# Kernel optimization log

Measured on AMD Instinct MI355X. Metric: run time of the kernel, lower is better.

Reference implementation:

```python
import jax, jax.numpy as jnp
import numpy as np

N_NODES = 50000
N_EDGES = 800000
IN_C, HID_C, OUT_C = 128, 128, 40


def gcn_conv(x, W, b, src, dst, dinv):
    # x: [N, Fin] -> [N, Fout]; PyG GCNConv: h = W x, then sym-normalized
    # aggregation over edges (incl. self-loops), plus bias.
    h = x @ W  # [N, Fout]
    norm = dinv[src] * dinv[dst]  # [E+N]
    msg = h[src] * norm[:, None]  # gather + scale, [E+N, Fout]
    out = jax.ops.segment_sum(msg, dst, num_segments=x.shape[0])
    return out + b


def _prep_edges(edge_index, n):
    # add self-loops; compute deg^{-1/2} with unit edge weights
    loop = jnp.arange(n, dtype=edge_index.dtype)
    src = jnp.concatenate([edge_index[0], loop])
    dst = jnp.concatenate([edge_index[1], loop])
    deg = jax.ops.segment_sum(jnp.ones_like(dst, dtype=jnp.float32), dst, num_segments=n)
    dinv = jnp.where(deg > 0, jax.lax.rsqrt(jnp.maximum(deg, 1.0)), 0.0)
    return src, dst, dinv


def setup_inputs() -> dict:
    key = jax.random.key(0)
    ks = jax.random.split(key, 5)
    x = jax.random.normal(ks[0], (N_NODES, IN_C), dtype=jnp.float32)
    edge_index = jax.random.randint(ks[1], (2, N_EDGES), 0, N_NODES, dtype=jnp.int32)
    s = 0.05
    W1 = jax.random.normal(ks[2], (IN_C, HID_C), dtype=jnp.float32) * s
    W2 = jax.random.normal(ks[3], (HID_C, HID_C), dtype=jnp.float32) * s
    W3 = jax.random.normal(ks[4], (HID_C, OUT_C), dtype=jnp.float32) * s
    return {
        "x": x, "edge_index": edge_index,
        "W1": W1, "b1": jnp.zeros((HID_C,), jnp.float32),
        "W2": W2, "b2": jnp.zeros((HID_C,), jnp.float32),
        "W3": W3, "b3": jnp.zeros((OUT_C,), jnp.float32),
    }


def reference(x, edge_index, W1, b1, W2, b2, W3, b3):
    n = x.shape[0]
    src, dst, dinv = _prep_edges(edge_index, n)
    h = jax.nn.relu(gcn_conv(x, W1, b1, src, dst, dinv))  # dropout = id (eval)
    h = jax.nn.relu(gcn_conv(h, W2, b2, src, dst, dinv))
    h = gcn_conv(h, W3, b3, src, dst, dinv)
    return jax.nn.log_softmax(h, axis=1)
```

## Files before the change

### kernel.cpp

```cpp
#include <hip/hip_runtime.h>
#include <cmath>

__device__ __forceinline__ unsigned short f2bf(float f) {
  unsigned u = __float_as_uint(f);
  u = (u + 0x7FFFu + ((u >> 16) & 1u)) >> 16;
  return (unsigned short)u;
}
__device__ __forceinline__ unsigned pack2(float a, float b) {
  return (unsigned)f2bf(a) | ((unsigned)f2bf(b) << 16);
}
__device__ __forceinline__ float bflo(unsigned u) { return __uint_as_float(u << 16); }
__device__ __forceinline__ float bfhi(unsigned u) { return __uint_as_float(u & 0xFFFF0000u); }
__device__ __forceinline__ float bf1(unsigned short h) { return __uint_as_float((unsigned)h << 16); }

__device__ __forceinline__ unsigned char fp8e(float v) {
  unsigned u = __float_as_uint(v * 0x1.0p-120f);
  unsigned s = (u >> 24) & 0x80u;
  u &= 0x7FFFFFFFu;
  u = u + 0x000FFFFFu + ((u >> 20) & 1u);
  return (unsigned char)(s | ((u >> 20) & 0x7Fu));
}
__device__ __forceinline__ float fp8d(unsigned b) {
  unsigned u = ((b & 0x80u) << 24) | ((b & 0x7Fu) << 20);
  return __uint_as_float(u) * 0x1.0p120f;
}

typedef float f32x2 __attribute__((ext_vector_type(2)));

#if defined(__has_builtin)
#if __has_builtin(__builtin_amdgcn_cvt_pk_f32_fp8)
#define HW_FP8 1
#endif
#endif

__device__ __forceinline__ void fp8d4(unsigned v, float4& acc) {
#ifdef HW_FP8
  f32x2 lo = __builtin_amdgcn_cvt_pk_f32_fp8((int)v, false);
  f32x2 hi = __builtin_amdgcn_cvt_pk_f32_fp8((int)v, true);
  acc.x += lo[0]; acc.y += lo[1]; acc.z += hi[0]; acc.w += hi[1];
#else
  acc.x += fp8d(v & 0xFF);
  acc.y += fp8d((v >> 8) & 0xFF);
  acc.z += fp8d((v >> 16) & 0xFF);
  acc.w += fp8d(v >> 24);
#endif
}

using bh8 = __attribute__((ext_vector_type(8))) short;
using f32x4 = __attribute__((ext_vector_type(4))) float;

#define BK_STRIDE 8192

__global__ __launch_bounds__(256) void k_bin(const int* __restrict__ src, const int* __restrict__ dst,
                                             int* __restrict__ bucketCur, unsigned* __restrict__ bucketBuf,
                                             int E, int chunk,
                                             const float* __restrict__ W1, const float* __restrict__ W2,
                                             const float* __restrict__ W3, unsigned short* __restrict__ Wt1,
                                             unsigned short* __restrict__ Wt2, unsigned short* __restrict__ Wt3) {
  __shared__ int hist[256], base[256], cur[256];
  int t = threadIdx.x;
  hist[t] = 0;
  cur[t] = 0;
  __syncthreads();
  int s0 = blockIdx.x * chunk;
  int s1 = min(E, s0 + chunk);
  for (int i = s0 + t; i < s1; i += 256) atomicAdd(&hist[dst[i] >> 8], 1);
  __syncthreads();
  if (hist[t] > 0) base[t] = atomicAdd(&bucketCur[t], hist[t]);
  __syncthreads();
  for (int i = s0 + t; i < s1; i += 256) {
    int d = dst[i];
    int b = d >> 8;
    int r = base[b] + atomicAdd(&cur[b], 1);
    if (r < BK_STRIDE)
      bucketBuf[(size_t)b * BK_STRIDE + r] = (unsigned)src[i] | ((unsigned)(d & 255) << 16);
  }
  int tid = blockIdx.x * 256 + t;
  int stride = gridDim.x * 256;
  for (int i = tid; i < 32768 + 6144; i += stride) {
    if (i < 16384) {
      int c = i >> 7, k = i & 127;
      Wt1[i] = f2bf(W1[(size_t)k * 128 + c]);
    } else if (i < 32768) {
      int j = i - 16384;
      int c = j >> 7, k = j & 127;
      Wt2[j] = f2bf(W2[(size_t)k * 128 + c]);
    } else {
      int j = i - 32768;
      int c = j >> 7, k = j & 127;
      Wt3[j] = (c < 40) ? f2bf(W3[(size_t)k * 40 + c]) : (unsigned short)0;
    }
  }
}

__global__ __launch_bounds__(256) void k_build(const unsigned* __restrict__ bucketBuf,
                                               const int* __restrict__ bucketCnt, int* __restrict__ rp,
                                               float* __restrict__ dinv, int* __restrict__ csr, int n, int nbk) {
  __shared__ int hist[256], excl[256], cur[256], s[256], bc[256];
  int b = blockIdx.x, t = threadIdx.x;
  int bv = (t < nbk) ? bucketCnt[t] : 0;
  bc[t] = bv;
  s[t] = bv;
  __syncthreads();
  for (int off = 1; off < 256; off <<= 1) {
    int u = (t >= off) ? s[t - off] : 0;
    __syncthreads();
    s[t] += u;
    __syncthreads();
  }
  int e0 = s[b] - bc[b];
  int cntE = bc[b];
  int Etot = s[nbk - 1];
  __syncthreads();
  const unsigned* buf = bucketBuf + (size_t)b * BK_STRIDE;
  hist[t] = 0;
  cur[t] = 0;
  __syncthreads();
  for (int i = t; i < cntE; i += 256) atomicAdd(&hist[(buf[i] >> 16) & 255], 1);
  __syncthreads();
  int h = hist[t];
  s[t] = h;
  __syncthreads();
  for (int off = 1; off < 256; off <<= 1) {
    int u = (t >= off) ? s[t - off] : 0;
    __syncthreads();
    s[t] += u;
    __syncthreads();
  }
  excl[t] = s[t] - h;
  int node = (b << 8) + t;
  if (node < n) {
    rp[node] = e0 + excl[t];
    dinv[node] = rsqrtf((float)(h + 1));
  }
  if (b == nbk - 1 && t == 0) rp[n] = Etot;
  __syncthreads();
  for (int i = t; i < cntE; i += 256) {
    unsigned p = buf[i];
    int lo = (p >> 16) & 255;
    int r = atomicAdd(&cur[lo], 1);
    csr[e0 + excl[lo] + r] = (int)(p & 0xFFFFu);
  }
}

template <int WT_N, int NW_COL, int MOUT, bool OUT8, bool A32>
__global__ __launch_bounds__(256) void k_mfma_gemm(const void* __restrict__ Av,
                                                   const unsigned short* __restrict__ Bt,
                                                   const float* __restrict__ dinv,
                                                   void* __restrict__ Gv, int n) {
  constexpr int NW_ROW = 4 / NW_COL;
  int tid = threadIdx.x;
  int wid = tid >> 6, lane = tid & 63;
  int lr = lane & 15, lq = lane >> 4;
  int wrow = wid / NW_COL, wcol = wid % NW_COL;
  int rowBase = blockIdx.x * (NW_ROW * 32) + wrow * 32;
  int colBase = wcol * (WT_N * 16);

  bh8 af[2][4];
#pragma unroll
  for (int rt = 0; rt < 2; rt++) {
    int row = rowBase + rt * 16 + lr;
    bool ok = row < n;
    if constexpr (A32) {
      const float* ap = (const float*)Av + (size_t)row * 128 + lq * 8;
#pragma unroll
      for (int ks = 0; ks < 4; ks++) {
        union { uint4 u; bh8 h; } w;
        if (ok) {
          float4 v0 = *(const float4*)(ap + ks * 32);
          float4 v1 = *(const float4*)(ap + ks * 32 + 4);
          w.u = make_uint4(pack2(v0.x, v0.y), pack2(v0.z, v0.w), pack2(v1.x, v1.y), pack2(v1.z, v1.w));
        } else {
          w.u = make_uint4(0u, 0u, 0u, 0u);
        }
        af[rt][ks] = w.h;
      }
    } else {
      const unsigned short* ap = (const unsigned short*)Av + (size_t)row * 128 + lq * 8;
#pragma unroll
      for (int ks = 0; ks < 4; ks++) {
        bh8 z = {0, 0, 0, 0, 0, 0, 0, 0};
        af[rt][ks] = ok ? *(const bh8*)(ap + ks * 32) : z;
      }
    }
  }
  bh8 bfr[WT_N][4];
#pragma unroll
  for (int ct = 0; ct < WT_N; ct++) {
    const unsigned short* bp = Bt + (size_t)(colBase + ct * 16 + lr) * 128 + lq * 8;
#pragma unroll
    for (int ks = 0; ks < 4; ks++) bfr[ct][ks] = *(const bh8*)(bp + ks * 32);
  }

  f32x4 acc[2][WT_N];
#pragma unroll
  for (int rt = 0; rt < 2; rt++)
#pragma unroll
    for (int ct = 0; ct < WT_N; ct++) acc[rt][ct] = (f32x4){0.f, 0.f, 0.f, 0.f};

#pragma unroll
  for (int ks = 0; ks < 4; ks++)
#pragma unroll
    for (int rt = 0; rt < 2; rt++)
#pragma unroll
      for (int ct = 0; ct < WT_N; ct++)
        acc[rt][ct] = __builtin_amdgcn_mfma_f32_16x16x32_bf16(af[rt][ks], bfr[ct][ks], acc[rt][ct], 0, 0, 0);

#pragma unroll
  for (int rt = 0; rt < 2; rt++)
#pragma unroll
    for (int r = 0; r < 4; r++) {
      int row = rowBase + rt * 16 + lq * 4 + r;
      if (row < n) {
        float di = dinv[row];
#pragma unroll
        for (int ct = 0; ct < WT_N; ct++) {
          int col = colBase + ct * 16 + lr;
          if (MOUT == 128 || col < MOUT) {
            if constexpr (OUT8)
              ((unsigned char*)Gv)[(size_t)row * MOUT + col] = fp8e(acc[rt][ct][r] * di);
            else
              ((unsigned short*)Gv)[(size_t)row * MOUT + col] = f2bf(acc[rt][ct][r] * di);
          }
        }
      }
    }
}

__global__ __launch_bounds__(256) void k_agg_relu128_f8(const unsigned char* __restrict__ g8,
                                                        const int* __restrict__ csr, const int* __restrict__ rp,
                                                        const float* __restrict__ dinv, const float* __restrict__ bias,
                                                        unsigned short* __restrict__ out, int n) {
  int t = threadIdx.x;
  int node = blockIdx.x * 8 + (t >> 5);
  if (node >= n) return;
  int c = t & 31;
  const unsigned* g32 = (const unsigned*)g8;
  int e0 = rp[node], e1 = rp[node + 1];

  float4 a[8];
#pragma unroll
  for (int u = 0; u < 8; u++) a[u] = make_float4(0.f, 0.f, 0.f, 0.f);
  fp8d4(g32[(size_t)node * 32 + c], a[0]);

  int e = e0;
  for (; e + 8 <= e1; e += 8) {
    int s[8];
#pragma unroll
    for (int u = 0; u < 8; u++) s[u] = csr[e + u];
    unsigned v[8];
#pragma unroll
    for (int u = 0; u < 8; u++) v[u] = g32[(size_t)s[u] * 32 + c];
#pragma unroll
    for (int u = 0; u < 8; u++) fp8d4(v[u], a[u]);
  }
  for (; e < e1; ++e) fp8d4(g32[(size_t)csr[e] * 32 + c], a[0]);

#pragma unroll
  for (int u = 4; u < 8; u++) {
    a[u - 4].x += a[u].x; a[u - 4].y += a[u].y; a[u - 4].z += a[u].z; a[u - 4].w += a[u].w;
  }
#pragma unroll
  for (int u = 2; u < 4; u++) {
    a[u - 2].x += a[u].x; a[u - 2].y += a[u].y; a[u - 2].z += a[u].z; a[u - 2].w += a[u].w;
  }
  float4 acc = make_float4(a[0].x + a[1].x, a[0].y + a[1].y, a[0].z + a[1].z, a[0].w + a[1].w);

  float di = dinv[node];
  float4 bb = *(const float4*)&bias[c * 4];
  uint2 o;
  o.x = pack2(fmaxf(fmaf(di, acc.x, bb.x), 0.f), fmaxf(fmaf(di, acc.y, bb.y), 0.f));
  o.y = pack2(fmaxf(fmaf(di, acc.z, bb.z), 0.f), fmaxf(fmaf(di, acc.w, bb.w), 0.f));
  *(uint2*)&out[(size_t)node * 128 + c * 4] = o;
}

__global__ __launch_bounds__(256) void k_agg_lsm40_f8(const unsigned char* __restrict__ g8,
                                                      const int* __restrict__ csr, const int* __restrict__ rp,
                                                      const float* __restrict__ dinv, const float* __restrict__ bias,
                                                      float* __restrict__ out, int n) {
  int lane = threadIdx.x & 63;
  int node = blockIdx.x * 4 + (threadIdx.x >> 6);
  if (node >= n) return;
  int e0 = rp[node], e1 = rp[node + 1];

  float a[8];
  a[0] = fp8d(g8[(size_t)node * 40 + lane]);
#pragma unroll
  for (int u = 1; u < 8; u++) a[u] = 0.f;

  int e = e0;
  for (; e + 8 <= e1; e += 8) {
    int s[8];
#pragma unroll
    for (int u = 0; u < 8; u++) s[u] = csr[e + u];
#pragma unroll
    for (int u = 0; u < 8; u++) a[u] += fp8d(g8[(size_t)s[u] * 40 + lane]);
  }
  for (; e < e1; ++e) a[0] += fp8d(g8[(size_t)csr[e] * 40 + lane]);

  float acc = ((a[0] + a[1]) + (a[2] + a[3])) + ((a[4] + a[5]) + (a[6] + a[7]));

  bool act = lane < 40;
  float v = act ? fmaf(dinv[node], acc, bias[lane]) : -INFINITY;
  float m = v;
#pragma unroll
  for (int off = 32; off > 0; off >>= 1) m = fmaxf(m, __shfl_xor(m, off, 64));
  float ex = act ? __expf(v - m) : 0.f;
  float ssum = ex;
#pragma unroll
  for (int off = 32; off > 0; off >>= 1) ssum += __shfl_xor(ssum, off, 64);
  if (act) out[(size_t)node * 40 + lane] = v - m - __logf(ssum);
}


extern "C" void kernel_launch(void* const* d_in, const int* in_sizes, int n_in,
                              void* d_out, int out_size, void* d_ws, size_t ws_size,
                              hipStream_t stream) {
  const float* x  = (const float*)d_in[0];
  const int*   ei = (const int*)d_in[1];
  const float* W1 = (const float*)d_in[2];
  const float* b1 = (const float*)d_in[3];
  const float* W2 = (const float*)d_in[4];
  const float* b2 = (const float*)d_in[5];
  const float* W3 = (const float*)d_in[6];
  const float* b3 = (const float*)d_in[7];
  float* out = (float*)d_out;
  int n = in_sizes[0] / 128;
  int E = in_sizes[1] / 2;
  const int* esrc = ei;
  const int* edst = ei + E;
  int nbk = (n + 255) >> 8;

  size_t off = 0;
  auto alloc = [&](size_t bytes) -> void* {
    void* r = (char*)d_ws + off;
    off += (bytes + 255) & ~(size_t)255;
    return r;
  };
  int*      bucketCur  = (int*)alloc(256 * 4);
  unsigned* bucketBuf  = (unsigned*)alloc((size_t)nbk * BK_STRIDE * 4);
  int*      rp         = (int*)alloc((size_t)(n + 1) * 4);
  float*    dinv       = (float*)alloc((size_t)n * 4);
  int*      csr        = (int*)alloc((size_t)E * 4);
  unsigned short* bufB = (unsigned short*)alloc((size_t)n * 128 * 2 + 4096);
  unsigned short* bufC = (unsigned short*)alloc((size_t)n * 128 * 2 + 4096);
  unsigned char*  gq   = (unsigned char*)alloc((size_t)n * 128 + 4096);
  unsigned short* Wt1  = (unsigned short*)alloc(128 * 128 * 2);
  unsigned short* Wt2  = (unsigned short*)alloc(128 * 128 * 2);
  unsigned short* Wt3  = (unsigned short*)alloc(48 * 128 * 2);

  hipMemsetAsync(bucketCur, 0, 256 * 4, stream);

  const int BIN_BLOCKS = 512;
  int chunk = (E + BIN_BLOCKS - 1) / BIN_BLOCKS;
  k_bin<<<BIN_BLOCKS, 256, 0, stream>>>(esrc, edst, bucketCur, bucketBuf, E, chunk, W1, W2, W3, Wt1, Wt2, Wt3);
  k_build<<<nbk, 256, 0, stream>>>(bucketBuf, bucketCur, rp, dinv, csr, n, nbk);

  k_mfma_gemm<4, 2, 128, true, true><<<(n + 63) / 64, 256, 0, stream>>>(x, Wt1, dinv, gq, n);
  k_agg_relu128_f8<<<(n + 7) / 8, 256, 0, stream>>>(gq, csr, rp, dinv, b1, bufB, n);
  k_mfma_gemm<4, 2, 128, true, false><<<(n + 63) / 64, 256, 0, stream>>>(bufB, Wt2, dinv, gq, n);
  k_agg_relu128_f8<<<(n + 7) / 8, 256, 0, stream>>>(gq, csr, rp, dinv, b2, bufC, n);
  k_mfma_gemm<3, 1, 40, true, false><<<(n + 127) / 128, 256, 0, stream>>>(bufC, Wt3, dinv, gq, n);
  k_agg_lsm40_f8<<<(n + 3) / 4, 256, 0, stream>>>(gq, csr, rp, dinv, b3, out, n);
}
```

Baseline: 180.8 us.

## Fuse aggregation with next-layer GEMM via LDS staging

Merges each layer's neighbour aggregation (bias and ReLU) with the following layer's MFMA GEMM. Each block aggregates 32 nodes into a padded LDS tile and multiplies it by the weight tile, so the bf16 hidden activations no longer go to global memory and two launches are removed. In exchange each block now does a serial gather phase followed by a GEMM phase with a barrier between them, and in the 40-column layer one of four waves sits idle during the GEMM, which may cost latency hiding.

After: 190.8 us. +5.5%, slower.

```diff
diff --git a/kernel.cpp b/kernel.cpp
--- a/kernel.cpp
+++ b/kernel.cpp
@@ -9,8 +9,6 @@
 __device__ __forceinline__ unsigned pack2(float a, float b) {
   return (unsigned)f2bf(a) | ((unsigned)f2bf(b) << 16);
 }
-__device__ __forceinline__ float bflo(unsigned u) { return __uint_as_float(u << 16); }
-__device__ __forceinline__ float bfhi(unsigned u) { return __uint_as_float(u & 0xFFFF0000u); }
 __device__ __forceinline__ float bf1(unsigned short h) { return __uint_as_float((unsigned)h << 16); }
 
 __device__ __forceinline__ unsigned char fp8e(float v) {
@@ -50,6 +48,7 @@
 using f32x4 = __attribute__((ext_vector_type(4))) float;
 
 #define BK_STRIDE 8192
+#define LDSW 136
 
 __global__ __launch_bounds__(256) void k_bin(const int* __restrict__ src, const int* __restrict__ dst,
                                              int* __restrict__ bucketCur, unsigned* __restrict__ bucketBuf,
@@ -143,45 +142,34 @@
   }
 }
 
-template <int WT_N, int NW_COL, int MOUT, bool OUT8, bool A32>
-__global__ __launch_bounds__(256) void k_mfma_gemm(const void* __restrict__ Av,
-                                                   const unsigned short* __restrict__ Bt,
-                                                   const float* __restrict__ dinv,
-                                                   void* __restrict__ Gv, int n) {
-  constexpr int NW_ROW = 4 / NW_COL;
+__global__ __launch_bounds__(256) void k_mfma_gemm1(const float* __restrict__ A, const unsigned short* __restrict__ Bt,
+                                                    const float* __restrict__ dinv, unsigned char* __restrict__ G,
+                                                    int n) {
+  constexpr int WT_N = 4;
   int tid = threadIdx.x;
   int wid = tid >> 6, lane = tid & 63;
   int lr = lane & 15, lq = lane >> 4;
-  int wrow = wid / NW_COL, wcol = wid % NW_COL;
-  int rowBase = blockIdx.x * (NW_ROW * 32) + wrow * 32;
-  int colBase = wcol * (WT_N * 16);
+  int wrow = wid >> 1, wcol = wid & 1;
+  int rowBase = blockIdx.x * 64 + wrow * 32;
+  int colBase = wcol * 64;
 
   bh8 af[2][4];
 #pragma unroll
   for (int rt = 0; rt < 2; rt++) {
     int row = rowBase + rt * 16 + lr;
     bool ok = row < n;
-    if constexpr (A32) {
-      const float* ap = (const float*)Av + (size_t)row * 128 + lq * 8;
-#pragma unroll
-      for (int ks = 0; ks < 4; ks++) {
-        union { uint4 u; bh8 h; } w;
-        if (ok) {
-          float4 v0 = *(const float4*)(ap + ks * 32);
-          float4 v1 = *(const float4*)(ap + ks * 32 + 4);
-          w.u = make_uint4(pack2(v0.x, v0.y), pack2(v0.z, v0.w), pack2(v1.x, v1.y), pack2(v1.z, v1.w));
-        } else {
-          w.u = make_uint4(0u, 0u, 0u, 0u);
-        }
-        af[rt][ks] = w.h;
-      }
-    } else {
-      const unsigned short* ap = (const unsigned short*)Av + (size_t)row * 128 + lq * 8;
-#pragma unroll
-      for (int ks = 0; ks < 4; ks++) {
-        bh8 z = {0, 0, 0, 0, 0, 0, 0, 0};
-        af[rt][ks] = ok ? *(const bh8*)(ap + ks * 32) : z;
-      }
+    const float* ap = A + (size_t)row * 128 + lq * 8;
+#pragma unroll
+    for (int ks = 0; ks < 4; ks++) {
+      union { uint4 u; bh8 h; } w;
+      if (ok) {
+        float4 v0 = *(const float4*)(ap + ks * 32);
+        float4 v1 = *(const float4*)(ap + ks * 32 + 4);
+        w.u = make_uint4(pack2(v0.x, v0.y), pack2(v0.z, v0.w), pack2(v1.x, v1.y), pack2(v1.z, v1.w));
+      } else {
+        w.u = make_uint4(0u, 0u, 0u, 0u);
+      }
+      af[rt][ks] = w.h;
     }
   }
   bh8 bfr[WT_N][4];
@@ -214,64 +202,114 @@
       if (row < n) {
         float di = dinv[row];
 #pragma unroll
+        for (int ct = 0; ct < WT_N; ct++)
+          G[(size_t)row * 128 + colBase + ct * 16 + lr] = fp8e(acc[rt][ct][r] * di);
+      }
+    }
+}
+
+template <int WT_N, int MOUT>
+__global__ __launch_bounds__(256) void k_fused_agg_gemm(const unsigned char* __restrict__ g8,
+                                                        const int* __restrict__ csr, const int* __restrict__ rp,
+                                                        const float* __restrict__ dinv, const float* __restrict__ bias,
+                                                        const unsigned short* __restrict__ Bt,
+                                                        unsigned char* __restrict__ Gout, int n) {
+  __shared__ unsigned short hs[32 * LDSW];
+  int t = threadIdx.x;
+  int rowBase = blockIdx.x * 32;
+
+  {
+    int c = t & 31;
+    const unsigned* g32 = (const unsigned*)g8;
+    float4 bb = *(const float4*)&bias[c * 4];
+    for (int u = 0; u < 4; u++) {
+      int nl = (t >> 5) + u * 8;
+      int node = rowBase + nl;
+      if (node >= n) continue;
+      int e0 = rp[node], e1 = rp[node + 1];
+      float4 a[8];
+#pragma unroll
+      for (int w = 0; w < 8; w++) a[w] = make_float4(0.f, 0.f, 0.f, 0.f);
+      fp8d4(g32[(size_t)node * 32 + c], a[0]);
+      int e = e0;
+      for (; e + 8 <= e1; e += 8) {
+        int s[8];
+#pragma unroll
+        for (int w = 0; w < 8; w++) s[w] = csr[e + w];
+        unsigned v[8];
+#pragma unroll
+        for (int w = 0; w < 8; w++) v[w] = g32[(size_t)s[w] * 32 + c];
+#pragma unroll
+        for (int w = 0; w < 8; w++) fp8d4(v[w], a[w]);
+      }
+      for (; e < e1; ++e) fp8d4(g32[(size_t)csr[e] * 32 + c], a[0]);
+#pragma unroll
+      for (int w = 4; w < 8; w++) {
+        a[w - 4].x += a[w].x; a[w - 4].y += a[w].y; a[w - 4].z += a[w].z; a[w - 4].w += a[w].w;
+      }
+#pragma unroll
+      for (int w = 2; w < 4; w++) {
+        a[w - 2].x += a[w].x; a[w - 2].y += a[w].y; a[w - 2].z += a[w].z; a[w - 2].w += a[w].w;
+      }
+      float4 acc = make_float4(a[0].x + a[1].x, a[0].y + a[1].y, a[0].z + a[1].z, a[0].w + a[1].w);
+      float di = dinv[node];
+      uint2 o;
+      o.x = pack2(fmaxf(fmaf(di, acc.x, bb.x), 0.f), fmaxf(fmaf(di, acc.y, bb.y), 0.f));
+      o.y = pack2(fmaxf(fmaf(di, acc.z, bb.z), 0.f), fmaxf(fmaf(di, acc.w, bb.w), 0.f));
+      *(uint2*)&hs[nl * LDSW + c * 4] = o;
+    }
+  }
+  __syncthreads();
+
+  int wid = t >> 6, lane = t & 63;
+  int lr = lane & 15, lq = lane >> 4;
+  int colBase = wid * (WT_N * 16);
+  if (MOUT == 40 && colBase >= 48) return;
+
+  bh8 af[2][4];
+#pragma unroll
+  for (int rt = 0; rt < 2; rt++)
+#pragma unroll
+    for (int ks = 0; ks < 4; ks++)
+      af[rt][ks] = *(const bh8*)&hs[(rt * 16 + lr) * LDSW + lq * 8 + ks * 32];
+
+  bh8 bfr[WT_N][4];
+#pragma unroll
+  for (int ct = 0; ct < WT_N; ct++) {
+    const unsigned short* bp = Bt + (size_t)(colBase + ct * 16 + lr) * 128 + lq * 8;
+#pragma unroll
+    for (int ks = 0; ks < 4; ks++) bfr[ct][ks] = *(const bh8*)(bp + ks * 32);
+  }
+
+  f32x4 acc[2][WT_N];
+#pragma unroll
+  for (int rt = 0; rt < 2; rt++)
+#pragma unroll
+    for (int ct = 0; ct < WT_N; ct++) acc[rt][ct] = (f32x4){0.f, 0.f, 0.f, 0.f};
+
+#pragma unroll
+  for (int ks = 0; ks < 4; ks++)
+#pragma unroll
+    for (int rt = 0; rt < 2; rt++)
+#pragma unroll
+      for (int ct = 0; ct < WT_N; ct++)
+        acc[rt][ct] = __builtin_amdgcn_mfma_f32_16x16x32_bf16(af[rt][ks], bfr[ct][ks], acc[rt][ct], 0, 0, 0);
+
+#pragma unroll
+  for (int rt = 0; rt < 2; rt++)
+#pragma unroll
+    for (int r = 0; r < 4; r++) {
+      int row = rowBase + rt * 16 + lq * 4 + r;
+      if (row < n) {
+        float di = dinv[row];
+#pragma unroll
         for (int ct = 0; ct < WT_N; ct++) {
           int col = colBase + ct * 16 + lr;
-          if (MOUT == 128 || col < MOUT) {
-            if constexpr (OUT8)
-              ((unsigned char*)Gv)[(size_t)row * MOUT + col] = fp8e(acc[rt][ct][r] * di);
-            else
-              ((unsigned short*)Gv)[(size_t)row * MOUT + col] = f2bf(acc[rt][ct][r] * di);
-          }
+          if (MOUT == 128 || col < MOUT)
+            Gout[(size_t)row * MOUT + col] = fp8e(acc[rt][ct][r] * di);
         }
       }
     }
-}
-
-__global__ __launch_bounds__(256) void k_agg_relu128_f8(const unsigned char* __restrict__ g8,
-                                                        const int* __restrict__ csr, const int* __restrict__ rp,
-                                                        const float* __restrict__ dinv, const float* __restrict__ bias,
-                                                        unsigned short* __restrict__ out, int n) {
-  int t = threadIdx.x;
-  int node = blockIdx.x * 8 + (t >> 5);
-  if (node >= n) return;
-  int c = t & 31;
-  const unsigned* g32 = (const unsigned*)g8;
-  int e0 = rp[node], e1 = rp[node + 1];
-
-  float4 a[8];
-#pragma unroll
-  for (int u = 0; u < 8; u++) a[u] = make_float4(0.f, 0.f, 0.f, 0.f);
-  fp8d4(g32[(size_t)node * 32 + c], a[0]);
-
-  int e = e0;
-  for (; e + 8 <= e1; e += 8) {
-    int s[8];
-#pragma unroll
-    for (int u = 0; u < 8; u++) s[u] = csr[e + u];
-    unsigned v[8];
-#pragma unroll
-    for (int u = 0; u < 8; u++) v[u] = g32[(size_t)s[u] * 32 + c];
-#pragma unroll
-    for (int u = 0; u < 8; u++) fp8d4(v[u], a[u]);
-  }
-  for (; e < e1; ++e) fp8d4(g32[(size_t)csr[e] * 32 + c], a[0]);
-
-#pragma unroll
-  for (int u = 4; u < 8; u++) {
-    a[u - 4].x += a[u].x; a[u - 4].y += a[u].y; a[u - 4].z += a[u].z; a[u - 4].w += a[u].w;
-  }
-#pragma unroll
-  for (int u = 2; u < 4; u++) {
-    a[u - 2].x += a[u].x; a[u - 2].y += a[u].y; a[u - 2].z += a[u].z; a[u - 2].w += a[u].w;
-  }
-  float4 acc = make_float4(a[0].x + a[1].x, a[0].y + a[1].y, a[0].z + a[1].z, a[0].w + a[1].w);
-
-  float di = dinv[node];
-  float4 bb = *(const float4*)&bias[c * 4];
-  uint2 o;
-  o.x = pack2(fmaxf(fmaf(di, acc.x, bb.x), 0.f), fmaxf(fmaf(di, acc.y, bb.y), 0.f));
-  o.y = pack2(fmaxf(fmaf(di, acc.z, bb.z), 0.f), fmaxf(fmaf(di, acc.w, bb.w), 0.f));
-  *(uint2*)&out[(size_t)node * 128 + c * 4] = o;
 }
 
 __global__ __launch_bounds__(256) void k_agg_lsm40_f8(const unsigned char* __restrict__ g8,
@@ -337,17 +375,16 @@
     off += (bytes + 255) & ~(size_t)255;
     return r;
   };
-  int*      bucketCur  = (int*)alloc(256 * 4);
-  unsigned* bucketBuf  = (unsigned*)alloc((size_t)nbk * BK_STRIDE * 4);
-  int*      rp         = (int*)alloc((size_t)(n + 1) * 4);
-  float*    dinv       = (float*)alloc((size_t)n * 4);
-  int*      csr        = (int*)alloc((size_t)E * 4);
-  unsigned short* bufB = (unsigned short*)alloc((size_t)n * 128 * 2 + 4096);
-  unsigned short* bufC = (unsigned short*)alloc((size_t)n * 128 * 2 + 4096);
-  unsigned char*  gq   = (unsigned char*)alloc((size_t)n * 128 + 4096);
-  unsigned short* Wt1  = (unsigned short*)alloc(128 * 128 * 2);
-  unsigned short* Wt2  = (unsigned short*)alloc(128 * 128 * 2);
-  unsigned short* Wt3  = (unsigned short*)alloc(48 * 128 * 2);
+  int*      bucketCur = (int*)alloc(256 * 4);
+  unsigned* bucketBuf = (unsigned*)alloc((size_t)nbk * BK_STRIDE * 4);
+  int*      rp        = (int*)alloc((size_t)(n + 1) * 4);
+  float*    dinv      = (float*)alloc((size_t)n * 4);
+  int*      csr       = (int*)alloc((size_t)E * 4);
+  unsigned char* gqA  = (unsigned char*)alloc((size_t)n * 128 + 4096);
+  unsigned char* gqB  = (unsigned char*)alloc((size_t)n * 128 + 4096);
+  unsigned short* Wt1 = (unsigned short*)alloc(128 * 128 * 2);
+  unsigned short* Wt2 = (unsigned short*)alloc(128 * 128 * 2);
+  unsigned short* Wt3 = (unsigned short*)alloc(48 * 128 * 2);
 
   hipMemsetAsync(bucketCur, 0, 256 * 4, stream);
 
@@ -356,10 +393,8 @@
   k_bin<<<BIN_BLOCKS, 256, 0, stream>>>(esrc, edst, bucketCur, bucketBuf, E, chunk, W1, W2, W3, Wt1, Wt2, Wt3);
   k_build<<<nbk, 256, 0, stream>>>(bucketBuf, bucketCur, rp, dinv, csr, n, nbk);
 
-  k_mfma_gemm<4, 2, 128, true, true><<<(n + 63) / 64, 256, 0, stream>>>(x, Wt1, dinv, gq, n);
-  k_agg_relu128_f8<<<(n + 7) / 8, 256, 0, stream>>>(gq, csr, rp, dinv, b1, bufB, n);
-  k_mfma_gemm<4, 2, 128, true, false><<<(n + 63) / 64, 256, 0, stream>>>(bufB, Wt2, dinv, gq, n);
-  k_agg_relu128_f8<<<(n + 7) / 8, 256, 0, stream>>>(gq, csr, rp, dinv, b2, bufC, n);
-  k_mfma_gemm<3, 1, 40, true, false><<<(n + 127) / 128, 256, 0, stream>>>(bufC, Wt3, dinv, gq, n);
-  k_agg_lsm40_f8<<<(n + 3) / 4, 256, 0, stream>>>(gq, csr, rp, dinv, b3, out, n);
-}
+  k_mfma_gemm1<<<(n + 63) / 64, 256, 0, stream>>>(x, Wt1, dinv, gqA, n);
+  k_fused_agg_gemm<2, 128><<<(n + 31) / 32, 256, 0, stream>>>(gqA, csr, rp, dinv, b1, Wt2, gqB, n);
+  k_fused_agg_gemm<1, 40><<<(n + 31) / 32, 256, 0, stream>>>(gqB, csr, rp, dinv, b2, Wt3, gqA, n);
+  k_agg_lsm40_f8<<<(n + 3) / 4, 256, 0, stream>>>(gqA, csr, rp, dinv, b3, out, n);
+}
```
